# Optimization experiments

Hardware: AMD Instinct MI355X
Metric: run time of the kernel (lower is better)

## Reference

```python
import jax, jax.numpy as jnp
import numpy as np

B, S, D, H = 2, 2048, 1024, 16
DK = D // H


def setup_inputs() -> dict:
    key = jax.random.key(0)
    ks = jax.random.split(key, 11)
    std = 1.0 / np.sqrt(D)
    inp = {
        "query": jax.random.normal(ks[0], (B, S, D), jnp.float32),
        "key": jax.random.normal(ks[1], (B, S, D), jnp.float32),
        "value": jax.random.normal(ks[2], (B, S, D), jnp.float32),
        # True = masked position (torch masked_fill semantics); causal mask
        "mask": jnp.triu(jnp.ones((1, 1, S, S), jnp.bool_), k=1),
        "Wq": jax.random.normal(ks[3], (D, D), jnp.float32) * std,
        "bq": jnp.zeros((D,), jnp.float32),
        "Wk": jax.random.normal(ks[4], (D, D), jnp.float32) * std,
        "bk": jnp.zeros((D,), jnp.float32),
        "Wv": jax.random.normal(ks[5], (D, D), jnp.float32) * std,
        "bv": jnp.zeros((D,), jnp.float32),
        "Wo": jax.random.normal(ks[6], (D, D), jnp.float32) * std,
        "bo": jnp.zeros((D,), jnp.float32),
    }
    return inp


def _split_heads(x):
    b, s, _ = x.shape
    return x.reshape(b, s, H, DK).transpose(0, 2, 1, 3)  # [b, H, s, dk]


def reference(query, key, value, mask, Wq, bq, Wk, bk, Wv, bv, Wo, bo):
    q = _split_heads(query @ Wq + bq)
    k = _split_heads(key @ Wk + bk)
    v = _split_heads(value @ Wv + bv)
    scale = 1.0 / (DK ** 0.5)
    logits = jnp.einsum("bhqd,bhkd->bhqk", q, k) * scale
    logits = jnp.where(mask, -1.0e9, logits)
    w = jax.nn.softmax(logits, axis=-1)
    att = jnp.einsum("bhqk,bhkd->bhqd", w, v)  # [B, H, S, dk]
    # NOTE: faithful to the original bug -- view() without permuting heads back,
    # i.e. a raw row-major reshape [B,H,S,dk] -> [B,S,H*dk].
    att = att.reshape(att.shape[0], att.shape[2], -1)
    out = att @ Wo + bo
    return out
```

## Files before the change

kernel.cpp:

```cpp
#include <hip/hip_runtime.h>
#include <hip/hip_bf16.h>

typedef __hip_bfloat16 bf16;
typedef __attribute__((ext_vector_type(8))) short bf16x8;
typedef __attribute__((ext_vector_type(4))) float f32x4;

constexpr int Bc  = 2;
constexpr int Sc  = 2048;
constexpr int Dc  = 1024;
constexpr int Hc  = 16;
constexpr int DKc = 64;

__device__ __forceinline__ float bfbits2f(unsigned short u) {
  return __uint_as_float(((unsigned)u) << 16);
}
__device__ __forceinline__ unsigned short f2bfbits(float x) {
  bf16 h = __float2bfloat16(x);
  return *reinterpret_cast<unsigned short*>(&h);
}
__device__ __forceinline__ void store1_dyn(char* base, size_t ei, int isf32, float v) {
  if (isf32) *reinterpret_cast<float*>(base + ei * 4) = v;
  else       *reinterpret_cast<bf16*>(base + ei * 2) = __float2bfloat16(v);
}
__device__ __forceinline__ float fast_exp2(float x) {
  return __builtin_amdgcn_exp2f(x);
}
__device__ __forceinline__ unsigned pkbf16(float a, float b) {
  __hip_bfloat162 h = __float22bfloat162_rn(make_float2(a, b));
  return *reinterpret_cast<unsigned*>(&h);
}
__device__ __forceinline__ uint4 pack8(const float4& a, const float4& b) {
  uint4 r;
  r.x = pkbf16(a.x, a.y);
  r.y = pkbf16(a.z, a.w);
  r.z = pkbf16(b.x, b.y);
  r.w = pkbf16(b.z, b.w);
  return r;
}
__device__ __forceinline__ void gld16(const void* g, void* l) {
  __builtin_amdgcn_global_load_lds(
      (const __attribute__((address_space(1))) unsigned int*)g,
      (__attribute__((address_space(3))) unsigned int*)l, 16, 0, 0);
}

__global__ __launch_bounds__(256)
void prep_all(const char* __restrict__ W0, const char* __restrict__ W1,
              const char* __restrict__ W2, const char* __restrict__ W3,
              unsigned short* __restrict__ Wt_all,
              const char* __restrict__ b0, const char* __restrict__ b1,
              const char* __restrict__ b2, const char* __restrict__ b3,
              unsigned short* __restrict__ bb_all,
              const char* __restrict__ A0, const char* __restrict__ A1,
              const char* __restrict__ A2, bf16* __restrict__ B0,
              bf16* __restrict__ B1, bf16* __restrict__ B2,
              int* __restrict__ flag_out) {
  __shared__ unsigned short T[64][72];
  __shared__ int cnt[256];
  const int id = blockIdx.x;
  const int tid = threadIdx.x;

  {
    const unsigned short* q = reinterpret_cast<const unsigned short*>(A0);
    int c = 0;
    for (int i = tid; i < 2048; i += 256) {
      const unsigned short u = q[i];
      const int e = (u >> 7) & 0xFF;
      if (e >= 134 || e <= 90) ++c;
    }
    cnt[tid] = c;
    __syncthreads();
    for (int s = 128; s > 0; s >>= 1) {
      if (tid < s) cnt[tid] += cnt[tid + s];
      __syncthreads();
    }
  }
  const int dyn = (cnt[0] > 64) ? 1 : 0;

  if (id < 1024) {
    const int z = id >> 8, rem = id & 255;
    const int n0 = (rem & 15) * 64, k0 = (rem >> 4) * 64;
    const char* W = (z == 0) ? W0 : (z == 1) ? W1 : (z == 2) ? W2 : W3;
    unsigned short* Wt = Wt_all + (size_t)z * Dc * Dc;
    const int r = tid >> 2, c16 = (tid & 3) * 16;

    unsigned short us[16];
    if (dyn) {
      const float4* p = reinterpret_cast<const float4*>(
          W + ((size_t)(k0 + r) * Dc + n0 + c16) * 4);
      const float4 f0 = p[0], f1 = p[1], f2 = p[2], f3 = p[3];
      const float fv[16] = {f0.x, f0.y, f0.z, f0.w, f1.x, f1.y, f1.z, f1.w,
                            f2.x, f2.y, f2.z, f2.w, f3.x, f3.y, f3.z, f3.w};
#pragma unroll
      for (int i = 0; i < 16; ++i) us[i] = f2bfbits(fv[i]);
    } else {
      const ushort4* p = reinterpret_cast<const ushort4*>(
          W + ((size_t)(k0 + r) * Dc + n0 + c16) * 2);
      const ushort4 u0 = p[0], u1 = p[1], u2 = p[2], u3 = p[3];
      us[0] = u0.x;  us[1] = u0.y;  us[2] = u0.z;  us[3] = u0.w;
      us[4] = u1.x;  us[5] = u1.y;  us[6] = u1.z;  us[7] = u1.w;
      us[8] = u2.x;  us[9] = u2.y;  us[10] = u2.z; us[11] = u2.w;
      us[12] = u3.x; us[13] = u3.y; us[14] = u3.z; us[15] = u3.w;
    }
#pragma unroll
    for (int i = 0; i < 16; ++i) T[r][c16 + i] = us[i];
    __syncthreads();

    unsigned vs[8];
#pragma unroll
    for (int i = 0; i < 8; ++i)
      vs[i] = (unsigned)T[c16 + 2 * i][r] | ((unsigned)T[c16 + 2 * i + 1][r] << 16);
    uint4* op = reinterpret_cast<uint4*>(Wt + (size_t)(n0 + r) * Dc + k0 + c16);
    op[0] = make_uint4(vs[0], vs[1], vs[2], vs[3]);
    op[1] = make_uint4(vs[4], vs[5], vs[6], vs[7]);
  } else if (id < 1028) {
    const int x = id - 1024;
    if (x == 0 && tid == 0) flag_out[0] = dyn;
    const char* src = (x == 0) ? b0 : (x == 1) ? b1 : (x == 2) ? b2 : b3;
    for (int i = tid; i < Dc; i += 256) {
      float v = dyn ? reinterpret_cast<const float*>(src)[i]
                    : bfbits2f(reinterpret_cast<const unsigned short*>(src)[i]);
      bb_all[x * Dc + i] = f2bfbits(v);
    }
  } else {
    const int j = id - 1028;
    const int z = j >> 9, x = j & 511;
    const char* src = (z == 0) ? A0 : (z == 1) ? A1 : A2;
    bf16* dst = (z == 0) ? B0 : (z == 1) ? B1 : B2;
    const size_t n = (size_t)4096 * Dc;
    const size_t stride = (size_t)512 * 256 * 8;
    for (size_t i = ((size_t)x * 256 + tid) * 8; i < n; i += stride) {
      uint4 u;
      if (dyn) {
        const float4* p = reinterpret_cast<const float4*>(src + i * 4);
        u = pack8(p[0], p[1]);
      } else {
        u = *reinterpret_cast<const uint4*>(src + i * 2);
      }
      *reinterpret_cast<uint4*>(dst + i) = u;
    }
  }
}

__global__ __launch_bounds__(256)
void qkv_gemm_async(const bf16* __restrict__ A0, const bf16* __restrict__ A1,
                    const bf16* __restrict__ A2,
                    const unsigned short* __restrict__ Wt_all,
                    const unsigned short* __restrict__ bias_all,
                    bf16* __restrict__ C0, bf16* __restrict__ C1,
                    bf16* __restrict__ C2) {
  constexpr int K = Dc, N = Dc;
  __shared__ __align__(16) unsigned short At[128 * 32];
  __shared__ __align__(16) unsigned short Bt[128 * 32];

  const int z = blockIdx.z;
  const bf16* A = (z == 0) ? A0 : (z == 1) ? A1 : A2;
  bf16* C = (z == 0) ? C0 : (z == 1) ? C1 : C2;
  const float scale = (z == 0) ? 0.18033688011112042f : 1.0f;
  const unsigned short* Wt = Wt_all + (size_t)z * Dc * Dc;
  const unsigned short* bias = bias_all + z * Dc;

  const int tid = threadIdx.x;
  const int m0 = blockIdx.x * 128, n0 = blockIdx.y * 128;
  const int w = tid >> 6, lane = tid & 63;
  const int lo16 = lane & 15, quad = lane >> 4;
  const int wm = (w >> 1) * 64, wn = (w & 1) * 64;

  unsigned short* ldsA = &At[w * 1024 + lane * 8];
  unsigned short* ldsB = &Bt[w * 1024 + lane * 8];
  const bf16* gA = A + (size_t)(m0 + w * 32 + (lane >> 2)) * K + (lane & 3) * 8;
  const unsigned short* gB = Wt + (size_t)(n0 + w * 32 + (lane >> 2)) * K + (lane & 3) * 8;

  f32x4 acc[4][4] = {};

  for (int k0 = 0; k0 < K; k0 += 32) {
    gld16(gA + k0, ldsA);
    gld16(gA + (size_t)16 * K + k0, ldsA + 512);
    gld16(gB + k0, ldsB);
    gld16(gB + (size_t)16 * K + k0, ldsB + 512);
    __syncthreads();

    bf16x8 afr[4], bfr[4];
#pragma unroll
    for (int mt = 0; mt < 4; ++mt)
      afr[mt] = *reinterpret_cast<const bf16x8*>(&At[(wm + mt * 16 + lo16) * 32 + quad * 8]);
#pragma unroll
    for (int nt = 0; nt < 4; ++nt)
      bfr[nt] = *reinterpret_cast<const bf16x8*>(&Bt[(wn + nt * 16 + lo16) * 32 + quad * 8]);
#pragma unroll
    for (int mt = 0; mt < 4; ++mt)
#pragma unroll
      for (int nt = 0; nt < 4; ++nt)
        acc[mt][nt] = __builtin_amdgcn_mfma_f32_16x16x32_bf16(afr[mt], bfr[nt],
                                                              acc[mt][nt], 0, 0, 0);
    __syncthreads();
  }

  float bv[4];
#pragma unroll
  for (int nt = 0; nt < 4; ++nt)
    bv[nt] = bfbits2f(bias[n0 + wn + nt * 16 + lo16]);
#pragma unroll
  for (int mt = 0; mt < 4; ++mt)
#pragma unroll
    for (int r = 0; r < 4; ++r) {
      const int row = m0 + wm + mt * 16 + quad * 4 + r;
#pragma unroll
      for (int nt = 0; nt < 4; ++nt) {
        const int col = n0 + wn + nt * 16 + lo16;
        C[(size_t)row * N + col] = __float2bfloat16((acc[mt][nt][r] + bv[nt]) * scale);
      }
    }
}

__global__ __launch_bounds__(256)
void qkv_gemm(const char* __restrict__ A0, const char* __restrict__ A1,
              const char* __restrict__ A2, const unsigned short* __restrict__ Wt_all,
              const unsigned short* __restrict__ bias_all,
              bf16* __restrict__ C0, bf16* __restrict__ C1, bf16* __restrict__ C2,
              const int* __restrict__ flagp) {
  constexpr int K = Dc, N = Dc;
  __shared__ __align__(16) unsigned short At[128][32];
  __shared__ __align__(16) unsigned short Bt[128][32];

  const int z = blockIdx.z;
  const char* A = (z == 0) ? A0 : (z == 1) ? A1 : A2;
  bf16* C = (z == 0) ? C0 : (z == 1) ? C1 : C2;
  const float scale = (z == 0) ? 0.18033688011112042f : 1.0f;
  const unsigned short* Wt = Wt_all + (size_t)z * Dc * Dc;
  const unsigned short* bias = bias_all + z * Dc;
  const int af = flagp[0];

  const int tid = threadIdx.x;
  const int m0 = blockIdx.x * 128, n0 = blockIdx.y * 128;
  const int w = tid >> 6, lane = tid & 63;
  const int lo16 = lane & 15, quad = lane >> 4;
  const int wm = (w >> 1) * 64, wn = (w & 1) * 64;
  const int sr = tid >> 1, sh = (tid & 1) * 16;

  f32x4 acc[4][4] = {};

  for (int k0 = 0; k0 < K; k0 += 32) {
    uint4 a_lo, a_hi;
    if (af) {
      const float4* p = reinterpret_cast<const float4*>(
          A + ((size_t)(m0 + sr) * K + k0 + sh) * 4);
      a_lo = pack8(p[0], p[1]);
      a_hi = pack8(p[2], p[3]);
    } else {
      const uint4* p = reinterpret_cast<const uint4*>(
          A + ((size_t)(m0 + sr) * K + k0 + sh) * 2);
      a_lo = p[0];
      a_hi = p[1];
    }
    const uint4* wp = reinterpret_cast<const uint4*>(Wt + (size_t)(n0 + sr) * K + k0 + sh);
    const uint4 b_lo = wp[0], b_hi = wp[1];

    __syncthreads();
    *reinterpret_cast<uint4*>(&At[sr][sh])     = a_lo;
    *reinterpret_cast<uint4*>(&At[sr][sh + 8]) = a_hi;
    *reinterpret_cast<uint4*>(&Bt[sr][sh])     = b_lo;
    *reinterpret_cast<uint4*>(&Bt[sr][sh + 8]) = b_hi;
    __syncthreads();

    bf16x8 afr[4], bfr[4];
#pragma unroll
    for (int mt = 0; mt < 4; ++mt)
      afr[mt] = *reinterpret_cast<const bf16x8*>(&At[wm + mt * 16 + lo16][quad * 8]);
#pragma unroll
    for (int nt = 0; nt < 4; ++nt)
      bfr[nt] = *reinterpret_cast<const bf16x8*>(&Bt[wn + nt * 16 + lo16][quad * 8]);
#pragma unroll
    for (int mt = 0; mt < 4; ++mt)
#pragma unroll
      for (int nt = 0; nt < 4; ++nt)
        acc[mt][nt] = __builtin_amdgcn_mfma_f32_16x16x32_bf16(afr[mt], bfr[nt],
                                                              acc[mt][nt], 0, 0, 0);
  }

  float bv[4];
#pragma unroll
  for (int nt = 0; nt < 4; ++nt)
    bv[nt] = bfbits2f(bias[n0 + wn + nt * 16 + lo16]);
#pragma unroll
  for (int mt = 0; mt < 4; ++mt)
#pragma unroll
    for (int r = 0; r < 4; ++r) {
      const int row = m0 + wm + mt * 16 + quad * 4 + r;
#pragma unroll
      for (int nt = 0; nt < 4; ++nt) {
        const int col = n0 + wn + nt * 16 + lo16;
        C[(size_t)row * N + col] = __float2bfloat16((acc[mt][nt][r] + bv[nt]) * scale);
      }
    }
}

__global__ __launch_bounds__(256)
void out_gemm_async(const bf16* __restrict__ A, const unsigned short* __restrict__ Wt,
                    const unsigned short* __restrict__ bias, char* __restrict__ C,
                    const int* __restrict__ flagp) {
  constexpr int K = Dc, N = Dc;
  __shared__ __align__(16) unsigned short At[128 * 32];
  __shared__ __align__(16) unsigned short Bt[128 * 32];

  const int cf = flagp[0];
  const int tid = threadIdx.x;
  const int m0 = blockIdx.x * 128, n0 = blockIdx.y * 128;
  const int w = tid >> 6, lane = tid & 63;
  const int lo16 = lane & 15, quad = lane >> 4;
  const int wm = (w >> 1) * 64, wn = (w & 1) * 64;

  unsigned short* ldsA = &At[w * 1024 + lane * 8];
  unsigned short* ldsB = &Bt[w * 1024 + lane * 8];
  const bf16* gA = A + (size_t)(m0 + w * 32 + (lane >> 2)) * K + (lane & 3) * 8;
  const unsigned short* gB = Wt + (size_t)(n0 + w * 32 + (lane >> 2)) * K + (lane & 3) * 8;

  f32x4 acc[4][4] = {};

  for (int k0 = 0; k0 < K; k0 += 32) {
    gld16(gA + k0, ldsA);
    gld16(gA + (size_t)16 * K + k0, ldsA + 512);
    gld16(gB + k0, ldsB);
    gld16(gB + (size_t)16 * K + k0, ldsB + 512);
    __syncthreads();

    bf16x8 afr[4], bfr[4];
#pragma unroll
    for (int mt = 0; mt < 4; ++mt)
      afr[mt] = *reinterpret_cast<const bf16x8*>(&At[(wm + mt * 16 + lo16) * 32 + quad * 8]);
#pragma unroll
    for (int nt = 0; nt < 4; ++nt)
      bfr[nt] = *reinterpret_cast<const bf16x8*>(&Bt[(wn + nt * 16 + lo16) * 32 + quad * 8]);
#pragma unroll
    for (int mt = 0; mt < 4; ++mt)
#pragma unroll
      for (int nt = 0; nt < 4; ++nt)
        acc[mt][nt] = __builtin_amdgcn_mfma_f32_16x16x32_bf16(afr[mt], bfr[nt],
                                                              acc[mt][nt], 0, 0, 0);
    __syncthreads();
  }

  float bv[4];
#pragma unroll
  for (int nt = 0; nt < 4; ++nt)
    bv[nt] = bfbits2f(bias[n0 + wn + nt * 16 + lo16]);
#pragma unroll
  for (int mt = 0; mt < 4; ++mt)
#pragma unroll
    for (int r = 0; r < 4; ++r) {
      const int row = m0 + wm + mt * 16 + quad * 4 + r;
#pragma unroll
      for (int nt = 0; nt < 4; ++nt) {
        const int col = n0 + wn + nt * 16 + lo16;
        store1_dyn(C, (size_t)row * N + col, cf, acc[mt][nt][r] + bv[nt]);
      }
    }
}

template <int SPLIT>
__global__ __launch_bounds__(256, 2)
void attn_mfma(const bf16* __restrict__ Q, const bf16* __restrict__ K,
               const bf16* __restrict__ V, bf16* __restrict__ O,
               float* __restrict__ P, float* __restrict__ Lp) {
  __shared__ __align__(16) unsigned short Kt[64][72];
  __shared__ __align__(16) unsigned short Vt[64][72];
  __shared__ __align__(16) unsigned short St[4][32][72];
  __shared__ float Li[4][32];

  const int hb = blockIdx.x & 31;
  int c, t0, t1, part;
  if constexpr (SPLIT) {
    const int u = blockIdx.x >> 5;
    if (u < 8)       { c = u;      t0 = 0;     t1 = 2 * c + 2; part = 0; }
    else if (u < 16) { c = 23 - u; t0 = 0;     t1 = c + 1;     part = 1; }
    else             { c = 31 - u; t0 = c + 1; t1 = 2 * c + 2; part = 2; }
  } else {
    const int i = blockIdx.x >> 5, g = i >> 3, r0 = i & 7;
    c = g ? (15 - r0) : r0; t0 = 0; t1 = 2 * (c + 1); part = 0;
  }
  const int b = hb >> 4, h = hb & 15;
  const int q0 = c * 128;
  const int tid = threadIdx.x;
  const int w = tid >> 6;
  const int lane = tid & 63;
  const int lo16 = lane & 15, quad = lane >> 4;
  const size_t hd = (size_t)h * DKc;

  const int kr = tid >> 2, kc = (tid & 3) * 16;
  const int vk = (tid & 31) * 2, vd0 = (tid >> 5) * 8;

  const bf16* qrowA = Q + ((size_t)(b * Sc + q0 + w * 32 + lo16)) * Dc + hd;
  const bf16x8 qa0 = *reinterpret_cast<const bf16x8*>(qrowA + quad * 8);
  const bf16x8 qa1 = *reinterpret_cast<const bf16x8*>(qrowA + 32 + quad * 8);
  const bf16* qrowB = qrowA + (size_t)16 * Dc;
  const bf16x8 qb0 = *reinterpret_cast<const bf16x8*>(qrowB + quad * 8);
  const bf16x8 qb1 = *reinterpret_cast<const bf16x8*>(qrowB + 32 + quad * 8);

  f32x4 oA[4] = {f32x4{0,0,0,0}, f32x4{0,0,0,0}, f32x4{0,0,0,0}, f32x4{0,0,0,0}};
  f32x4 oB[4] = {f32x4{0,0,0,0}, f32x4{0,0,0,0}, f32x4{0,0,0,0}, f32x4{0,0,0,0}};
  float lsA = 0.f, lsB = 0.f;
  const int qgA = q0 + w * 32 + lo16;
  const int qgB = qgA + 16;
  const int qmaxA = q0 + w * 32 + 15;
  const int qmaxB = qmaxA + 16;

  const bf16* ksrc = K + ((size_t)(b * Sc + kr)) * Dc + hd + kc;
  const bf16* vsrc = V + ((size_t)(b * Sc + vk)) * Dc + hd + vd0;

  const size_t off0 = (size_t)t0 * 64 * Dc;
  uint4 rKa = *reinterpret_cast<const uint4*>(ksrc + off0);
  uint4 rKb = *reinterpret_cast<const uint4*>(ksrc + off0 + 8);
  uint4 rVa = *reinterpret_cast<const uint4*>(vsrc + off0);
  uint4 rVb = *reinterpret_cast<const uint4*>(vsrc + off0 + Dc);

  for (int t = t0; t < t1; ++t) {
    const int kt = t * 64;
    __syncthreads();
    *reinterpret_cast<uint4*>(&Kt[kr][kc])     = rKa;
    *reinterpret_cast<uint4*>(&Kt[kr][kc + 8]) = rKb;
    *reinterpret_cast<unsigned*>(&Vt[vd0 + 0][vk]) = (rVa.x & 0xffffu) | (rVb.x << 16);
    *reinterpret_cast<unsigned*>(&Vt[vd0 + 1][vk]) = (rVa.x >> 16)     | (rVb.x & 0xffff0000u);
    *reinterpret_cast<unsigned*>(&Vt[vd0 + 2][vk]) = (rVa.y & 0xffffu) | (rVb.y << 16);
    *reinterpret_cast<unsigned*>(&Vt[vd0 + 3][vk]) = (rVa.y >> 16)     | (rVb.y & 0xffff0000u);
    *reinterpret_cast<unsigned*>(&Vt[vd0 + 4][vk]) = (rVa.z & 0xffffu) | (rVb.z << 16);
    *reinterpret_cast<unsigned*>(&Vt[vd0 + 5][vk]) = (rVa.z >> 16)     | (rVb.z & 0xffff0000u);
    *reinterpret_cast<unsigned*>(&Vt[vd0 + 6][vk]) = (rVa.w & 0xffffu) | (rVb.w << 16);
    *reinterpret_cast<unsigned*>(&Vt[vd0 + 7][vk]) = (rVa.w >> 16)     | (rVb.w & 0xffff0000u);
    __syncthreads();

    if (t + 1 < t1) {
      const size_t off = (size_t)(t + 1) * 64 * Dc;
      rKa = *reinterpret_cast<const uint4*>(ksrc + off);
      rKb = *reinterpret_cast<const uint4*>(ksrc + off + 8);
      rVa = *reinterpret_cast<const uint4*>(vsrc + off);
      rVb = *reinterpret_cast<const uint4*>(vsrc + off + Dc);
    }

    if (kt > qmaxB) continue;
    const bool liveA = (kt <= qmaxA);

    bf16x8 ka[4], kb[4];
#pragma unroll
    for (int ct = 0; ct < 4; ++ct) {
      ka[ct] = *reinterpret_cast<const bf16x8*>(&Kt[ct * 16 + lo16][quad * 8]);
      kb[ct] = *reinterpret_cast<const bf16x8*>(&Kt[ct * 16 + lo16][32 + quad * 8]);
    }

    f32x4 sA[4] = {f32x4{0,0,0,0}, f32x4{0,0,0,0}, f32x4{0,0,0,0}, f32x4{0,0,0,0}};
    f32x4 sB[4] = {f32x4{0,0,0,0}, f32x4{0,0,0,0}, f32x4{0,0,0,0}, f32x4{0,0,0,0}};
    __builtin_amdgcn_s_setprio(1);
#pragma unroll
    for (int ct = 0; ct < 4; ++ct) {
      sB[ct] = __builtin_amdgcn_mfma_f32_16x16x32_bf16(ka[ct], qb0, sB[ct], 0, 0, 0);
      sB[ct] = __builtin_amdgcn_mfma_f32_16x16x32_bf16(kb[ct], qb1, sB[ct], 0, 0, 0);
    }
    if (liveA) {
#pragma unroll
      for (int ct = 0; ct < 4; ++ct) {
        sA[ct] = __builtin_amdgcn_mfma_f32_16x16x32_bf16(ka[ct], qa0, sA[ct], 0, 0, 0);
        sA[ct] = __builtin_amdgcn_mfma_f32_16x16x32_bf16(kb[ct], qa1, sA[ct], 0, 0, 0);
      }
    }
    __builtin_amdgcn_s_setprio(0);

    if (kt + 63 > q0 + w * 32 + 16) {
#pragma unroll
      for (int ct = 0; ct < 4; ++ct)
#pragma unroll
        for (int r = 0; r < 4; ++r)
          if (kt + ct * 16 + quad * 4 + r > qgB) sB[ct][r] = -1e9f;
    }
    if (liveA && (kt + 63 > q0 + w * 32)) {
#pragma unroll
      for (int ct = 0; ct < 4; ++ct)
#pragma unroll
        for (int r = 0; r < 4; ++r)
          if (kt + ct * 16 + quad * 4 + r > qgA) sA[ct][r] = -1e9f;
    }

#pragma unroll
    for (int ct = 0; ct < 4; ++ct) {
      const float p0 = fast_exp2(sB[ct][0]);
      const float p1 = fast_exp2(sB[ct][1]);
      const float p2 = fast_exp2(sB[ct][2]);
      const float p3 = fast_exp2(sB[ct][3]);
      lsB += (p0 + p1) + (p2 + p3);
      uint2 pk;
      pk.x = pkbf16(p0, p1);
      pk.y = pkbf16(p2, p3);
      *reinterpret_cast<uint2*>(&St[w][16 + lo16][ct * 16 + quad * 4]) = pk;
    }
    if (liveA) {
#pragma unroll
      for (int ct = 0; ct < 4; ++ct) {
        const float p0 = fast_exp2(sA[ct][0]);
        const float p1 = fast_exp2(sA[ct][1]);
        const float p2 = fast_exp2(sA[ct][2]);
        const float p3 = fast_exp2(sA[ct][3]);
        lsA += (p0 + p1) + (p2 + p3);
        uint2 pk;
        pk.x = pkbf16(p0, p1);
        pk.y = pkbf16(p2, p3);
        *reinterpret_cast<uint2*>(&St[w][lo16][ct * 16 + quad * 4]) = pk;
      }
    }

    const bf16x8 pb0 = *reinterpret_cast<const bf16x8*>(&St[w][16 + lo16][quad * 8]);
    const bf16x8 pb1 = *reinterpret_cast<const bf16x8*>(&St[w][16 + lo16][32 + quad * 8]);
    const bf16x8 pa0 = *reinterpret_cast<const bf16x8*>(&St[w][lo16][quad * 8]);
    const bf16x8 pa1 = *reinterpret_cast<const bf16x8*>(&St[w][lo16][32 + quad * 8]);
    __builtin_amdgcn_s_setprio(1);
#pragma unroll
    for (int ct = 0; ct < 4; ++ct) {
      const bf16x8 vb0 = *reinterpret_cast<const bf16x8*>(&Vt[ct * 16 + lo16][quad * 8]);
      const bf16x8 vb1 = *reinterpret_cast<const bf16x8*>(&Vt[ct * 16 + lo16][32 + quad * 8]);
      oB[ct] = __builtin_amdgcn_mfma_f32_16x16x32_bf16(pb0, vb0, oB[ct], 0, 0, 0);
      oB[ct] = __builtin_amdgcn_mfma_f32_16x16x32_bf16(pb1, vb1, oB[ct], 0, 0, 0);
      if (liveA) {
        oA[ct] = __builtin_amdgcn_mfma_f32_16x16x32_bf16(pa0, vb0, oA[ct], 0, 0, 0);
        oA[ct] = __builtin_amdgcn_mfma_f32_16x16x32_bf16(pa1, vb1, oA[ct], 0, 0, 0);
      }
    }
    __builtin_amdgcn_s_setprio(0);
  }

  lsA += __shfl_xor(lsA, 16);
  lsA += __shfl_xor(lsA, 32);
  lsB += __shfl_xor(lsB, 16);
  lsB += __shfl_xor(lsB, 32);

  if (SPLIT && part != 0) {
    float* Pp = P + ((size_t)(part - 1) * 32 + hb) * (size_t)(1024 * 64);
    float* Lq = Lp + ((size_t)(part - 1) * 32 + hb) * 1024;
    const int qlA = q0 - 1024 + w * 32;
    if (quad == 0) {
      Lq[qlA + lo16] = lsA;
      Lq[qlA + 16 + lo16] = lsB;
    }
#pragma unroll
    for (int r = 0; r < 4; ++r) {
      float* pA = Pp + (size_t)(qlA + quad * 4 + r) * 64 + lo16;
      float* pB = Pp + (size_t)(qlA + 16 + quad * 4 + r) * 64 + lo16;
#pragma unroll
      for (int ct = 0; ct < 4; ++ct) {
        pA[ct * 16] = oA[ct][r];
        pB[ct * 16] = oB[ct][r];
      }
    }
    return;
  }

  if (quad == 0) {
    Li[w][lo16] = 1.f / lsA;
    Li[w][16 + lo16] = 1.f / lsB;
  }
  __builtin_amdgcn_wave_barrier();
  const f32x4 invA = *reinterpret_cast<const f32x4*>(&Li[w][quad * 4]);
  const f32x4 invB = *reinterpret_cast<const f32x4*>(&Li[w][16 + quad * 4]);

#pragma unroll
  for (int r = 0; r < 4; ++r) {
    bf16* opA = O + (((size_t)(b * Hc + h) * Sc) + q0 + w * 32 + quad * 4 + r) * DKc + lo16;
    bf16* opB = opA + (size_t)16 * DKc;
#pragma unroll
    for (int ct = 0; ct < 4; ++ct) {
      opA[ct * 16] = __float2bfloat16(oA[ct][r] * invA[r]);
      opB[ct * 16] = __float2bfloat16(oB[ct][r] * invB[r]);
    }
  }
}

__global__ __launch_bounds__(256)
void merge_att(const float* __restrict__ P, const float* __restrict__ Lp,
               bf16* __restrict__ att) {
  const int e = blockIdx.x * 256 + threadIdx.x;
  const int d4 = (e & 15) * 4;
  const int q  = (e >> 4) & 1023;
  const int hb = e >> 14;
  const size_t pi = ((size_t)hb * 1024 + q) * 64 + d4;
  const float4 a = *reinterpret_cast<const float4*>(P + pi);
  const float4 c = *reinterpret_cast<const float4*>(P + (size_t)2097152 + pi);
  const float inv = 1.f / (Lp[hb * 1024 + q] + Lp[32768 + hb * 1024 + q]);
  uint2 o;
  o.x = pkbf16((a.x + c.x) * inv, (a.y + c.y) * inv);
  o.y = pkbf16((a.z + c.z) * inv, (a.w + c.w) * inv);
  *reinterpret_cast<uint2*>(att + ((size_t)hb * 2048 + 1024 + q) * 64 + d4) = o;
}

extern "C" void kernel_launch(void* const* d_in, const int* in_sizes, int n_in,
                              void* d_out, int out_size, void* d_ws, size_t ws_size,
                              hipStream_t stream) {
  (void)in_sizes; (void)out_size;
  const char* query = (const char*)d_in[0];
  const char* key_  = (const char*)d_in[1];
  const char* value = (const char*)d_in[2];
  const int wb = n_in - 8;
  const char* Wq = (const char*)d_in[wb + 0];
  const char* bq = (const char*)d_in[wb + 1];
  const char* Wk = (const char*)d_in[wb + 2];
  const char* bk = (const char*)d_in[wb + 3];
  const char* Wv = (const char*)d_in[wb + 4];
  const char* bv = (const char*)d_in[wb + 5];
  const char* Wo = (const char*)d_in[wb + 6];
  const char* bo = (const char*)d_in[wb + 7];

  char* ws = (char*)d_ws;
  bf16* Qs  = (bf16*)(ws);
  bf16* Ks  = (bf16*)(ws + ((size_t)8  << 20));
  bf16* Vs  = (bf16*)(ws + ((size_t)16 << 20));
  bf16* att = (bf16*)(ws + ((size_t)24 << 20));
  unsigned short* Wt_all = (unsigned short*)(ws + ((size_t)32 << 20));
  unsigned short* bb_all = (unsigned short*)(ws + ((size_t)40 << 20));
  int* flag = (int*)(ws + ((size_t)40 << 20) + 16384);
  bf16* Qb = (bf16*)(ws + ((size_t)42 << 20));
  bf16* Kb = (bf16*)(ws + ((size_t)50 << 20));
  bf16* Vb = (bf16*)(ws + ((size_t)58 << 20));
  float* Pw = (float*)(ws + ((size_t)42 << 20));
  float* Lw = (float*)(ws + ((size_t)59 << 20));
  const bool big_ws = ws_size >= ((size_t)66 << 20);

  if (big_ws) {
    prep_all<<<2564, 256, 0, stream>>>(Wq, Wk, Wv, Wo, Wt_all, bq, bk, bv, bo,
                                       bb_all, query, key_, value, Qb, Kb, Vb, flag);
    qkv_gemm_async<<<dim3(32, 8, 3), 256, 0, stream>>>(Qb, Kb, Vb, Wt_all, bb_all,
                                                       Qs, Ks, Vs);
    attn_mfma<1><<<dim3(768), 256, 0, stream>>>(Qs, Ks, Vs, att, Pw, Lw);
    merge_att<<<dim3(2048), 256, 0, stream>>>(Pw, Lw, att);
  } else {
    prep_all<<<1028, 256, 0, stream>>>(Wq, Wk, Wv, Wo, Wt_all, bq, bk, bv, bo,
                                       bb_all, query, key_, value,
                                       (bf16*)att, (bf16*)att, (bf16*)att, flag);
    qkv_gemm<<<dim3(32, 8, 3), 256, 0, stream>>>(query, key_, value, Wt_all, bb_all,
                                                 Qs, Ks, Vs, flag);
    attn_mfma<0><<<dim3(512), 256, 0, stream>>>(Qs, Ks, Vs, att, Pw, Lw);
  }

  out_gemm_async<<<dim3(32, 8), 256, 0, stream>>>(att, Wt_all + (size_t)3 * Dc * Dc,
                                                  bb_all + 3 * Dc, (char*)d_out, flag);
}
```

Measured before the change: 226.6 us.

## Double GEMM K-tile to 64 with XOR-swizzled LDS layout

In both the QKV and output projection GEMMs, the K step per iteration grows from 32 to 64, which halves the number of barrier pairs and gives each barrier two MFMA k-substeps. The LDS tiles become 128x64, and the column chunk each global-to-LDS load writes is XOR-swizzled by row so that fragment reads avoid bank conflicts with the wider row stride. LDS use per block doubles, which may lower occupancy, and there is still no double buffering.

Measured after the change: 229.3 us. About the same (+1.2%).

```diff
diff --git a/kernel.cpp b/kernel.cpp
--- a/kernel.cpp
+++ b/kernel.cpp
@@ -149,8 +149,8 @@
                     bf16* __restrict__ C0, bf16* __restrict__ C1,
                     bf16* __restrict__ C2) {
   constexpr int K = Dc, N = Dc;
-  __shared__ __align__(16) unsigned short At[128 * 32];
-  __shared__ __align__(16) unsigned short Bt[128 * 32];
+  __shared__ __align__(16) unsigned short At[128 * 64];
+  __shared__ __align__(16) unsigned short Bt[128 * 64];
 
   const int z = blockIdx.z;
   const bf16* A = (z == 0) ? A0 : (z == 1) ? A1 : A2;
@@ -165,33 +165,43 @@
   const int lo16 = lane & 15, quad = lane >> 4;
   const int wm = (w >> 1) * 64, wn = (w & 1) * 64;
 
-  unsigned short* ldsA = &At[w * 1024 + lane * 8];
-  unsigned short* ldsB = &Bt[w * 1024 + lane * 8];
-  const bf16* gA = A + (size_t)(m0 + w * 32 + (lane >> 2)) * K + (lane & 3) * 8;
-  const unsigned short* gB = Wt + (size_t)(n0 + w * 32 + (lane >> 2)) * K + (lane & 3) * 8;
+  unsigned short* ldsA = &At[w * 2048 + lane * 8];
+  unsigned short* ldsB = &Bt[w * 2048 + lane * 8];
+  const int ssw = ((lane & 7) ^ (lane >> 3)) * 8;
+  const bf16* gA = A + (size_t)(m0 + w * 32 + (lane >> 3)) * K + ssw;
+  const unsigned short* gB = Wt + (size_t)(n0 + w * 32 + (lane >> 3)) * K + ssw;
+
+  const int rsw = (lo16 & 7) << 3;
+  const int c0 = (quad * 8) ^ rsw;
+  const int c1 = (32 + quad * 8) ^ rsw;
 
   f32x4 acc[4][4] = {};
 
-  for (int k0 = 0; k0 < K; k0 += 32) {
-    gld16(gA + k0, ldsA);
-    gld16(gA + (size_t)16 * K + k0, ldsA + 512);
-    gld16(gB + k0, ldsB);
-    gld16(gB + (size_t)16 * K + k0, ldsB + 512);
-    __syncthreads();
-
-    bf16x8 afr[4], bfr[4];
-#pragma unroll
-    for (int mt = 0; mt < 4; ++mt)
-      afr[mt] = *reinterpret_cast<const bf16x8*>(&At[(wm + mt * 16 + lo16) * 32 + quad * 8]);
-#pragma unroll
-    for (int nt = 0; nt < 4; ++nt)
-      bfr[nt] = *reinterpret_cast<const bf16x8*>(&Bt[(wn + nt * 16 + lo16) * 32 + quad * 8]);
-#pragma unroll
-    for (int mt = 0; mt < 4; ++mt)
+  for (int k0 = 0; k0 < K; k0 += 64) {
+#pragma unroll
+    for (int r = 0; r < 4; ++r) {
+      gld16(gA + (size_t)(r * 8) * K + k0, ldsA + r * 512);
+      gld16(gB + (size_t)(r * 8) * K + k0, ldsB + r * 512);
+    }
+    __syncthreads();
+
+#pragma unroll
+    for (int kk = 0; kk < 2; ++kk) {
+      const int cc = kk ? c1 : c0;
+      bf16x8 afr[4], bfr[4];
+#pragma unroll
+      for (int mt = 0; mt < 4; ++mt)
+        afr[mt] = *reinterpret_cast<const bf16x8*>(&At[(wm + mt * 16 + lo16) * 64 + cc]);
 #pragma unroll
       for (int nt = 0; nt < 4; ++nt)
-        acc[mt][nt] = __builtin_amdgcn_mfma_f32_16x16x32_bf16(afr[mt], bfr[nt],
-                                                              acc[mt][nt], 0, 0, 0);
+        bfr[nt] = *reinterpret_cast<const bf16x8*>(&Bt[(wn + nt * 16 + lo16) * 64 + cc]);
+#pragma unroll
+      for (int mt = 0; mt < 4; ++mt)
+#pragma unroll
+        for (int nt = 0; nt < 4; ++nt)
+          acc[mt][nt] = __builtin_amdgcn_mfma_f32_16x16x32_bf16(afr[mt], bfr[nt],
+                                                                acc[mt][nt], 0, 0, 0);
+    }
     __syncthreads();
   }
 
@@ -299,8 +309,8 @@
                     const unsigned short* __restrict__ bias, char* __restrict__ C,
                     const int* __restrict__ flagp) {
   constexpr int K = Dc, N = Dc;
-  __shared__ __align__(16) unsigned short At[128 * 32];
-  __shared__ __align__(16) unsigned short Bt[128 * 32];
+  __shared__ __align__(16) unsigned short At[128 * 64];
+  __shared__ __align__(16) unsigned short Bt[128 * 64];
 
   const int cf = flagp[0];
   const int tid = threadIdx.x;
@@ -309,33 +319,43 @@
   const int lo16 = lane & 15, quad = lane >> 4;
   const int wm = (w >> 1) * 64, wn = (w & 1) * 64;
 
-  unsigned short* ldsA = &At[w * 1024 + lane * 8];
-  unsigned short* ldsB = &Bt[w * 1024 + lane * 8];
-  const bf16* gA = A + (size_t)(m0 + w * 32 + (lane >> 2)) * K + (lane & 3) * 8;
-  const unsigned short* gB = Wt + (size_t)(n0 + w * 32 + (lane >> 2)) * K + (lane & 3) * 8;
+  unsigned short* ldsA = &At[w * 2048 + lane * 8];
+  unsigned short* ldsB = &Bt[w * 2048 + lane * 8];
+  const int ssw = ((lane & 7) ^ (lane >> 3)) * 8;
+  const bf16* gA = A + (size_t)(m0 + w * 32 + (lane >> 3)) * K + ssw;
+  const unsigned short* gB = Wt + (size_t)(n0 + w * 32 + (lane >> 3)) * K + ssw;
+
+  const int rsw = (lo16 & 7) << 3;
+  const int c0 = (quad * 8) ^ rsw;
+  const int c1 = (32 + quad * 8) ^ rsw;
 
   f32x4 acc[4][4] = {};
 
-  for (int k0 = 0; k0 < K; k0 += 32) {
-    gld16(gA + k0, ldsA);
-    gld16(gA + (size_t)16 * K + k0, ldsA + 512);
-    gld16(gB + k0, ldsB);
-    gld16(gB + (size_t)16 * K + k0, ldsB + 512);
-    __syncthreads();
-
-    bf16x8 afr[4], bfr[4];
-#pragma unroll
-    for (int mt = 0; mt < 4; ++mt)
-      afr[mt] = *reinterpret_cast<const bf16x8*>(&At[(wm + mt * 16 + lo16) * 32 + quad * 8]);
-#pragma unroll
-    for (int nt = 0; nt < 4; ++nt)
-      bfr[nt] = *reinterpret_cast<const bf16x8*>(&Bt[(wn + nt * 16 + lo16) * 32 + quad * 8]);
-#pragma unroll
-    for (int mt = 0; mt < 4; ++mt)
+  for (int k0 = 0; k0 < K; k0 += 64) {
+#pragma unroll
+    for (int r = 0; r < 4; ++r) {
+      gld16(gA + (size_t)(r * 8) * K + k0, ldsA + r * 512);
+      gld16(gB + (size_t)(r * 8) * K + k0, ldsB + r * 512);
+    }
+    __syncthreads();
+
+#pragma unroll
+    for (int kk = 0; kk < 2; ++kk) {
+      const int cc = kk ? c1 : c0;
+      bf16x8 afr[4], bfr[4];
+#pragma unroll
+      for (int mt = 0; mt < 4; ++mt)
+        afr[mt] = *reinterpret_cast<const bf16x8*>(&At[(wm + mt * 16 + lo16) * 64 + cc]);
 #pragma unroll
       for (int nt = 0; nt < 4; ++nt)
-        acc[mt][nt] = __builtin_amdgcn_mfma_f32_16x16x32_bf16(afr[mt], bfr[nt],
-                                                              acc[mt][nt], 0, 0, 0);
+        bfr[nt] = *reinterpret_cast<const bf16x8*>(&Bt[(wn + nt * 16 + lo16) * 64 + cc]);
+#pragma unroll
+      for (int mt = 0; mt < 4; ++mt)
+#pragma unroll
+        for (int nt = 0; nt < 4; ++nt)
+          acc[mt][nt] = __builtin_amdgcn_mfma_f32_16x16x32_bf16(afr[mt], bfr[nt],
+                                                                acc[mt][nt], 0, 0, 0);
+    }
     __syncthreads();
   }
 
```

## Fuse input fp32-to-bf16 conversion into QKV GEMM A-tile loads

Applied to the files above, without the earlier changes.

Drops the separate prep pass that converted query/key/value to bf16 in workspace. The QKV GEMM now reads the raw inputs directly, converts them in registers and writes swizzled bf16 tiles to LDS. The K-step grows from 32 to 64, and the next A tile is prefetched into registers while the current one computes. This removes a full write and re-read of the converted activations, at the cost of register-staged A loads in place of async global-to-LDS loads, plus extra conversion work repeated across the N-dimension blocks.

After: 276.4 us. 1.22x slower.

```diff
diff --git a/kernel.cpp b/kernel.cpp
--- a/kernel.cpp
+++ b/kernel.cpp
@@ -50,9 +50,7 @@
               const char* __restrict__ b0, const char* __restrict__ b1,
               const char* __restrict__ b2, const char* __restrict__ b3,
               unsigned short* __restrict__ bb_all,
-              const char* __restrict__ A0, const char* __restrict__ A1,
-              const char* __restrict__ A2, bf16* __restrict__ B0,
-              bf16* __restrict__ B1, bf16* __restrict__ B2,
+              const char* __restrict__ A0,
               int* __restrict__ flag_out) {
   __shared__ unsigned short T[64][72];
   __shared__ int cnt[256];
@@ -112,7 +110,7 @@
     uint4* op = reinterpret_cast<uint4*>(Wt + (size_t)(n0 + r) * Dc + k0 + c16);
     op[0] = make_uint4(vs[0], vs[1], vs[2], vs[3]);
     op[1] = make_uint4(vs[4], vs[5], vs[6], vs[7]);
-  } else if (id < 1028) {
+  } else {
     const int x = id - 1024;
     if (x == 0 && tid == 0) flag_out[0] = dyn;
     const char* src = (x == 0) ? b0 : (x == 1) ? b1 : (x == 2) ? b2 : b3;
@@ -121,43 +119,27 @@
                     : bfbits2f(reinterpret_cast<const unsigned short*>(src)[i]);
       bb_all[x * Dc + i] = f2bfbits(v);
     }
-  } else {
-    const int j = id - 1028;
-    const int z = j >> 9, x = j & 511;
-    const char* src = (z == 0) ? A0 : (z == 1) ? A1 : A2;
-    bf16* dst = (z == 0) ? B0 : (z == 1) ? B1 : B2;
-    const size_t n = (size_t)4096 * Dc;
-    const size_t stride = (size_t)512 * 256 * 8;
-    for (size_t i = ((size_t)x * 256 + tid) * 8; i < n; i += stride) {
-      uint4 u;
-      if (dyn) {
-        const float4* p = reinterpret_cast<const float4*>(src + i * 4);
-        u = pack8(p[0], p[1]);
-      } else {
-        u = *reinterpret_cast<const uint4*>(src + i * 2);
-      }
-      *reinterpret_cast<uint4*>(dst + i) = u;
-    }
   }
 }
 
 __global__ __launch_bounds__(256)
-void qkv_gemm_async(const bf16* __restrict__ A0, const bf16* __restrict__ A1,
-                    const bf16* __restrict__ A2,
+void qkv_gemm_async(const char* __restrict__ A0, const char* __restrict__ A1,
+                    const char* __restrict__ A2,
                     const unsigned short* __restrict__ Wt_all,
                     const unsigned short* __restrict__ bias_all,
                     bf16* __restrict__ C0, bf16* __restrict__ C1,
-                    bf16* __restrict__ C2) {
+                    bf16* __restrict__ C2, const int* __restrict__ flagp) {
   constexpr int K = Dc, N = Dc;
-  __shared__ __align__(16) unsigned short At[128 * 32];
-  __shared__ __align__(16) unsigned short Bt[128 * 32];
+  __shared__ __align__(16) unsigned short At[128 * 64];
+  __shared__ __align__(16) unsigned short Bt[128 * 64];
 
   const int z = blockIdx.z;
-  const bf16* A = (z == 0) ? A0 : (z == 1) ? A1 : A2;
+  const char* A = (z == 0) ? A0 : (z == 1) ? A1 : A2;
   bf16* C = (z == 0) ? C0 : (z == 1) ? C1 : C2;
   const float scale = (z == 0) ? 0.18033688011112042f : 1.0f;
   const unsigned short* Wt = Wt_all + (size_t)z * Dc * Dc;
   const unsigned short* bias = bias_all + z * Dc;
+  const int af = flagp[0];
 
   const int tid = threadIdx.x;
   const int m0 = blockIdx.x * 128, n0 = blockIdx.y * 128;
@@ -165,34 +147,66 @@
   const int lo16 = lane & 15, quad = lane >> 4;
   const int wm = (w >> 1) * 64, wn = (w & 1) * 64;
 
-  unsigned short* ldsA = &At[w * 1024 + lane * 8];
-  unsigned short* ldsB = &Bt[w * 1024 + lane * 8];
-  const bf16* gA = A + (size_t)(m0 + w * 32 + (lane >> 2)) * K + (lane & 3) * 8;
-  const unsigned short* gB = Wt + (size_t)(n0 + w * 32 + (lane >> 2)) * K + (lane & 3) * 8;
+  const int sr = tid >> 1, sh = (tid & 1) * 32;
+  const int swr = (sr & 7) << 3;
+
+  unsigned short* ldsB = &Bt[w * 2048 + lane * 8];
+  const int ssw = ((lane & 7) ^ (lane >> 3)) * 8;
+  const unsigned short* gB = Wt + (size_t)(n0 + w * 32 + (lane >> 3)) * K + ssw;
+
+  const int rsw = (lo16 & 7) << 3;
+  const int c0 = (quad * 8) ^ rsw;
+  const int c1 = (32 + quad * 8) ^ rsw;
 
   f32x4 acc[4][4] = {};
 
-  for (int k0 = 0; k0 < K; k0 += 32) {
-    gld16(gA + k0, ldsA);
-    gld16(gA + (size_t)16 * K + k0, ldsA + 512);
-    gld16(gB + k0, ldsB);
-    gld16(gB + (size_t)16 * K + k0, ldsB + 512);
-    __syncthreads();
-
-    bf16x8 afr[4], bfr[4];
-#pragma unroll
-    for (int mt = 0; mt < 4; ++mt)
-      afr[mt] = *reinterpret_cast<const bf16x8*>(&At[(wm + mt * 16 + lo16) * 32 + quad * 8]);
-#pragma unroll
-    for (int nt = 0; nt < 4; ++nt)
-      bfr[nt] = *reinterpret_cast<const bf16x8*>(&Bt[(wn + nt * 16 + lo16) * 32 + quad * 8]);
-#pragma unroll
-    for (int mt = 0; mt < 4; ++mt)
+  uint4 ua[4];
+  auto loadA = [&](int k0) {
+#pragma unroll
+    for (int j = 0; j < 4; ++j) {
+      const int c = sh + j * 8;
+      if (af) {
+        const float4* p = reinterpret_cast<const float4*>(
+            A + ((size_t)(m0 + sr) * K + k0 + c) * 4);
+        ua[j] = pack8(p[0], p[1]);
+      } else {
+        ua[j] = *reinterpret_cast<const uint4*>(
+            A + ((size_t)(m0 + sr) * K + k0 + c) * 2);
+      }
+    }
+  };
+
+  loadA(0);
+
+  for (int k0 = 0; k0 < K; k0 += 64) {
+    __syncthreads();
+#pragma unroll
+    for (int j = 0; j < 4; ++j)
+      *reinterpret_cast<uint4*>(&At[sr * 64 + ((sh + j * 8) ^ swr)]) = ua[j];
+#pragma unroll
+    for (int r = 0; r < 4; ++r)
+      gld16(gB + (size_t)(r * 8) * K + k0, ldsB + r * 512);
+    __syncthreads();
+
+    if (k0 + 64 < K) loadA(k0 + 64);
+
+#pragma unroll
+    for (int kk = 0; kk < 2; ++kk) {
+      const int cc = kk ? c1 : c0;
+      bf16x8 afr[4], bfr[4];
+#pragma unroll
+      for (int mt = 0; mt < 4; ++mt)
+        afr[mt] = *reinterpret_cast<const bf16x8*>(&At[(wm + mt * 16 + lo16) * 64 + cc]);
 #pragma unroll
       for (int nt = 0; nt < 4; ++nt)
-        acc[mt][nt] = __builtin_amdgcn_mfma_f32_16x16x32_bf16(afr[mt], bfr[nt],
-                                                              acc[mt][nt], 0, 0, 0);
-    __syncthreads();
+        bfr[nt] = *reinterpret_cast<const bf16x8*>(&Bt[(wn + nt * 16 + lo16) * 64 + cc]);
+#pragma unroll
+      for (int mt = 0; mt < 4; ++mt)
+#pragma unroll
+        for (int nt = 0; nt < 4; ++nt)
+          acc[mt][nt] = __builtin_amdgcn_mfma_f32_16x16x32_bf16(afr[mt], bfr[nt],
+                                                                acc[mt][nt], 0, 0, 0);
+    }
   }
 
   float bv[4];
@@ -611,24 +625,20 @@
   unsigned short* Wt_all = (unsigned short*)(ws + ((size_t)32 << 20));
   unsigned short* bb_all = (unsigned short*)(ws + ((size_t)40 << 20));
   int* flag = (int*)(ws + ((size_t)40 << 20) + 16384);
-  bf16* Qb = (bf16*)(ws + ((size_t)42 << 20));
-  bf16* Kb = (bf16*)(ws + ((size_t)50 << 20));
-  bf16* Vb = (bf16*)(ws + ((size_t)58 << 20));
   float* Pw = (float*)(ws + ((size_t)42 << 20));
   float* Lw = (float*)(ws + ((size_t)59 << 20));
   const bool big_ws = ws_size >= ((size_t)66 << 20);
 
+  prep_all<<<1028, 256, 0, stream>>>(Wq, Wk, Wv, Wo, Wt_all, bq, bk, bv, bo,
+                                     bb_all, query, flag);
+
   if (big_ws) {
-    prep_all<<<2564, 256, 0, stream>>>(Wq, Wk, Wv, Wo, Wt_all, bq, bk, bv, bo,
-                                       bb_all, query, key_, value, Qb, Kb, Vb, flag);
-    qkv_gemm_async<<<dim3(32, 8, 3), 256, 0, stream>>>(Qb, Kb, Vb, Wt_all, bb_all,
-                                                       Qs, Ks, Vs);
+    qkv_gemm_async<<<dim3(32, 8, 3), 256, 0, stream>>>(query, key_, value,
+                                                       Wt_all, bb_all,
+                                                       Qs, Ks, Vs, flag);
     attn_mfma<1><<<dim3(768), 256, 0, stream>>>(Qs, Ks, Vs, att, Pw, Lw);
     merge_att<<<dim3(2048), 256, 0, stream>>>(Pw, Lw, att);
   } else {
-    prep_all<<<1028, 256, 0, stream>>>(Wq, Wk, Wv, Wo, Wt_all, bq, bk, bv, bo,
-                                       bb_all, query, key_, value,
-                                       (bf16*)att, (bf16*)att, (bf16*)att, flag);
     qkv_gemm<<<dim3(32, 8, 3), 256, 0, stream>>>(query, key_, value, Wt_all, bb_all,
                                                  Qs, Ks, Vs, flag);
     attn_mfma<0><<<dim3(512), 256, 0, stream>>>(Qs, Ks, Vs, att, Pw, Lw);
```
